# Kernel optimization log

Measured on AMD Instinct MI355X. Metric: run time of the kernel, lower is better.

Reference implementation:

```python
import jax, jax.numpy as jnp
import numpy as np

B, C, H, W = 4, 256, 64, 64
CH = C // 2  # inner channels


def setup_inputs() -> dict:
    key = jax.random.key(0)
    ks = jax.random.split(key, 9)
    s = 1.0 / np.sqrt(C)
    so = 1.0 / np.sqrt(CH)
    return {
        "x": jax.random.normal(ks[0], (B, C, H, W), dtype=jnp.float32),
        "teta_w": jax.random.uniform(ks[1], (CH, C), jnp.float32, -s, s),
        "teta_b": jax.random.uniform(ks[2], (CH,), jnp.float32, -s, s),
        "fi_w": jax.random.uniform(ks[3], (CH, C), jnp.float32, -s, s),
        "fi_b": jax.random.uniform(ks[4], (CH,), jnp.float32, -s, s),
        "gi_w": jax.random.uniform(ks[5], (CH, C), jnp.float32, -s, s),
        "gi_b": jax.random.uniform(ks[6], (CH,), jnp.float32, -s, s),
        "out_w": jax.random.uniform(ks[7], (C, CH), jnp.float32, -so, so),
        "out_b": jax.random.uniform(ks[8], (C,), jnp.float32, -so, so),
    }


def _conv1x1(x, w, b):
    # x: (B, Cin, H, W), w: (Cout, Cin) -> (B, Cout, H, W)
    return jnp.einsum('bchw,oc->bohw', x, w) + b[None, :, None, None]


def reference(x, teta_w, teta_b, fi_w, fi_b, gi_w, gi_b, out_w, out_b):
    b, c, h, w = x.shape
    n = h * w
    ch = teta_w.shape[0]
    # NOTE: original uses .view (reshape), NOT transpose, to get (B, N, Ch)
    x1 = _conv1x1(x, teta_w, teta_b).reshape(b, ch, n).reshape(b, n, ch)
    x2 = _conv1x1(x, fi_w, fi_b).reshape(b, ch, n)            # (B, Ch, N)
    x3 = _conv1x1(x, gi_w, gi_b).reshape(b, ch, n).reshape(b, n, ch)
    # softmax over dim=1 (rows), as in the original
    attn = jax.nn.softmax(jnp.matmul(x1, x2), axis=1)          # (B, N, N)
    y = jnp.matmul(attn, x3)                                   # (B, N, Ch)
    y = jnp.swapaxes(y, 1, 2).reshape(b, ch, h, w)
    return x + _conv1x1(y, out_w, out_b)
```

## Files before the change

### kernel.cpp

```cpp
#include <hip/hip_runtime.h>
#include <hip/hip_bf16.h>

#define BB 4
#define CC 256
#define CHH 128
#define NN 4096
#define KSHIFT 12.0f

typedef __attribute__((ext_vector_type(8))) short bf16x8;
typedef __attribute__((ext_vector_type(4))) float f32x4;

__device__ __forceinline__ float to_f(float v) { return v; }
__device__ __forceinline__ float to_f(__hip_bfloat16 v) { return __bfloat162float(v); }
__device__ __forceinline__ void st_f(float* p, float v) { *p = v; }
__device__ __forceinline__ void st_f(__hip_bfloat16* p, float v) { *p = __float2bfloat16(v); }
__device__ __forceinline__ unsigned short f2bf(float f) {
    __hip_bfloat16 h = __float2bfloat16(f);
    unsigned short u;
    __builtin_memcpy(&u, &h, 2);
    return u;
}
__device__ __forceinline__ bf16x8 ldb8(const unsigned short* p) { return *(const bf16x8*)p; }

__device__ __forceinline__ void gload_lds16(const unsigned short* g, unsigned short* l) {
    __builtin_amdgcn_global_load_lds(
        (const __attribute__((address_space(1))) unsigned int*)g,
        (__attribute__((address_space(3))) unsigned int*)l, 16, 0, 0);
}

__global__ void detect_kernel(const void* __restrict__ tb, int* __restrict__ flag) {
    if (threadIdx.x == 0) {
        const __hip_bfloat16* p = (const __hip_bfloat16*)tb;
        int big = 0, zeros = 0;
        for (int i = 0; i < 128; ++i) {
            float v = __bfloat162float(p[i]);
            if (!(fabsf(v) <= 0.5f)) big = 1;
            if ((i & 1) == 0 && v == 0.0f) zeros++;
        }
        *flag = (big || zeros >= 32) ? 1 : 0;
    }
}

template <typename T>
__device__ __forceinline__ void prep_body(const T* tw, const T* fw, const T* gw, const T* ow,
                                          const T* tb2, const T* fb, const T* gb, const T* ob,
                                          unsigned short* Wb, unsigned short* OWb,
                                          float* Bf, float* OBf) {
    int idx = blockIdx.x * 256 + threadIdx.x;
    if (idx < 98304) {
        int cv = idx >> 15, rem = idx & 32767;
        const T* src = cv == 0 ? tw : (cv == 1 ? fw : gw);
        Wb[idx] = f2bf(to_f(src[rem]));
    } else if (idx < 131072) {
        OWb[idx - 98304] = f2bf(to_f(ow[idx - 98304]));
    } else if (idx < 131456) {
        int r = idx - 131072;
        int cv = r >> 7, j = r & 127;
        const T* src = cv == 0 ? tb2 : (cv == 1 ? fb : gb);
        Bf[r] = to_f(src[j]);
    } else if (idx < 131712) {
        OBf[idx - 131456] = to_f(ob[idx - 131456]);
    }
}

__global__ void prep_kernel(const void* tw, const void* fw, const void* gw, const void* ow,
                            const void* tb2, const void* fb, const void* gb, const void* ob,
                            const int* __restrict__ flag,
                            unsigned short* Wb, unsigned short* OWb, float* Bf, float* OBf) {
    if (*flag)
        prep_body<float>((const float*)tw, (const float*)fw, (const float*)gw, (const float*)ow,
                         (const float*)tb2, (const float*)fb, (const float*)gb, (const float*)ob,
                         Wb, OWb, Bf, OBf);
    else
        prep_body<__hip_bfloat16>((const __hip_bfloat16*)tw, (const __hip_bfloat16*)fw,
                                  (const __hip_bfloat16*)gw, (const __hip_bfloat16*)ow,
                                  (const __hip_bfloat16*)tb2, (const __hip_bfloat16*)fb,
                                  (const __hip_bfloat16*)gb, (const __hip_bfloat16*)ob,
                                  Wb, OWb, Bf, OBf);
}

template <typename T>
__device__ __forceinline__ void xtrans_body(const T* __restrict__ x, unsigned short* __restrict__ xt) {
    int b = blockIdx.z;
    const T* in = x + (size_t)b * CC * NN;
    unsigned short* out = xt + (size_t)b * NN * CC;
    int p0 = blockIdx.x * 64, c0 = blockIdx.y * 64;
    __shared__ unsigned short t[64][68];
    int flat = threadIdx.x;
#pragma unroll
    for (int tt = 0; tt < 16; ++tt) {
        int id = flat + tt * 256;
        int rr = id >> 6, cc = id & 63;
        t[cc][rr] = f2bf(to_f(in[(size_t)(c0 + rr) * NN + p0 + cc]));
    }
    __syncthreads();
#pragma unroll
    for (int tt = 0; tt < 16; ++tt) {
        int id = flat + tt * 256;
        int pp = id >> 6, jj = id & 63;
        out[(size_t)(p0 + pp) * CC + c0 + jj] = t[pp][jj];
    }
}

__launch_bounds__(256)
__global__ void xtrans_kernel(const void* x, const int* __restrict__ flag,
                              unsigned short* __restrict__ xt) {
    if (*flag) xtrans_body<float>((const float*)x, xt);
    else       xtrans_body<__hip_bfloat16>((const __hip_bfloat16*)x, xt);
}

__launch_bounds__(256)
__global__ void conv3_mfma_kernel(const unsigned short* __restrict__ xt,
                                  const unsigned short* __restrict__ Wb,
                                  const float* __restrict__ Bf,
                                  unsigned short* __restrict__ T1b,
                                  unsigned short* __restrict__ T2t,
                                  unsigned short* __restrict__ T3b) {
    int b = blockIdx.y;
    int p0 = blockIdx.x * 16;
    int flat = threadIdx.x;
    int w = flat >> 6, lane = flat & 63, m = lane & 15, quad = lane >> 4;
    const unsigned short* xrow = xt + ((size_t)b * NN + p0 + m) * CC;
    bf16x8 xf[8];
#pragma unroll
    for (int kc = 0; kc < 8; ++kc)
        xf[kc] = ldb8(&xrow[kc * 32 + quad * 8]);
    unsigned short* t1  = T1b + (size_t)b * CHH * NN;
    unsigned short* t2t = T2t + (size_t)b * CHH * NN;
    unsigned short* t3  = T3b + (size_t)b * CHH * NN;
#pragma unroll
    for (int q = 0; q < 6; ++q) {
        int t = w * 6 + q;
        int cv = t >> 3, ot = t & 7;
        int o0 = ot * 16;
        const unsigned short* wrow = Wb + ((size_t)cv * CHH + o0 + m) * CC;
        f32x4 acc = {0.f, 0.f, 0.f, 0.f};
#pragma unroll
        for (int kc = 0; kc < 8; ++kc) {
            bf16x8 wf = ldb8(&wrow[kc * 32 + quad * 8]);
            acc = __builtin_amdgcn_mfma_f32_16x16x32_bf16(wf, xf[kc], acc, 0, 0, 0);
        }
        unsigned short hv[4];
#pragma unroll
        for (int r = 0; r < 4; ++r)
            hv[r] = f2bf(acc[r] + Bf[cv * CHH + o0 + quad * 4 + r]);
        if (cv == 1) {
            unsigned int lo = (unsigned int)hv[0] | ((unsigned int)hv[1] << 16);
            unsigned int hi = (unsigned int)hv[2] | ((unsigned int)hv[3] << 16);
            int src = (lane & 3) * 16 + (lane >> 2);
            unsigned int tlo = (unsigned int)__shfl((int)lo, src, 64);
            unsigned int thi = (unsigned int)__shfl((int)hi, src, 64);
            unsigned int* dst = (unsigned int*)&t2t[(size_t)(p0 + (lane >> 2)) * CHH +
                                                    o0 + (lane & 3) * 4];
            dst[0] = tlo;
            dst[1] = thi;
        } else {
            unsigned short* outp = (cv == 0) ? t1 : t3;
#pragma unroll
            for (int r = 0; r < 4; ++r)
                outp[(size_t)(o0 + quad * 4 + r) * NN + p0 + m] = hv[r];
        }
    }
}

__launch_bounds__(256)
__global__ void transpose_kernel(const unsigned short* __restrict__ in,
                                 unsigned short* __restrict__ out, int R, int C) {
    int bz = blockIdx.z;
    in  += (size_t)bz * R * C;
    out += (size_t)bz * R * C;
    int c0 = blockIdx.x * 64, r0 = blockIdx.y * 64;
    __shared__ unsigned short t[64][68];
    int flat = threadIdx.x;
#pragma unroll
    for (int tt = 0; tt < 16; ++tt) {
        int id = flat + tt * 256;
        int r = id >> 6, c = id & 63;
        t[c][r] = in[(size_t)(r0 + r) * C + c0 + c];
    }
    __syncthreads();
#pragma unroll
    for (int tt = 0; tt < 16; ++tt) {
        int id = flat + tt * 256;
        int c = id >> 6, r = id & 63;
        out[(size_t)(c0 + c) * R + r0 + r] = t[c][r];
    }
}

__launch_bounds__(256)
__global__ void stats_mfma_kernel(const unsigned short* __restrict__ T1b,
                                  const unsigned short* __restrict__ T2t,
                                  float* __restrict__ Lpart) {
    int blk = blockIdx.x;
    int b = (blk & 7) >> 1;
    int rest = (blk >> 3) * 2 + (blk & 1);
    int strip = rest >> 3, iq = rest & 7;
    int ibase = iq * 512;
    int flat = threadIdx.x;
    int w = flat >> 6, lane = flat & 63, m = lane & 15, quad = lane >> 4;
    const unsigned short* A  = T1b + (size_t)b * CHH * NN;
    const unsigned short* Bt = T2t + (size_t)b * CHH * NN;
    __shared__ unsigned short th[2][64 * 128];

    int u0w = strip * 128 + w * 32;
    bf16x8 bfr[2][4];
#pragma unroll
    for (int g = 0; g < 2; ++g)
#pragma unroll
        for (int kc = 0; kc < 4; ++kc)
            bfr[g][kc] = ldb8(&Bt[(size_t)(u0w + g * 16 + m) * CHH + kc * 32 + quad * 8]);

#define STAGE_TH(dst, ii)                                                          \
    _Pragma("unroll")                                                              \
    for (int i_ = 0; i_ < 4; ++i_) {                                               \
        int sl = i_ * 256 + flat;                                                  \
        int r_ = sl >> 4, ch_ = sl & 15;                                           \
        int c_ = ch_ ^ (r_ & 7);                                                   \
        gload_lds16(&A[(size_t)((ii) + r_) * CHH + c_ * 8], &th[dst][sl * 8]);     \
    }

    float csum[2] = {0.f, 0.f};
    STAGE_TH(0, ibase);
    __syncthreads();
    int cur = 0;
    for (int t = 0; t < 8; ++t) {
        if (t < 7) { STAGE_TH(cur ^ 1, ibase + (t + 1) * 64); }
        const unsigned short* thc = th[cur];
#pragma unroll
        for (int s = 0; s < 4; ++s) {
            int irow = s * 16 + m;
            bf16x8 af[4];
#pragma unroll
            for (int kc = 0; kc < 4; ++kc) {
                int ch = (kc * 4 + quad) ^ (irow & 7);
                af[kc] = *(const bf16x8*)&thc[irow * 128 + ch * 8];
            }
#pragma unroll
            for (int g = 0; g < 2; ++g) {
                f32x4 acc = {0.f, 0.f, 0.f, 0.f};
#pragma unroll
                for (int kc = 0; kc < 4; ++kc)
                    acc = __builtin_amdgcn_mfma_f32_16x16x32_bf16(af[kc], bfr[g][kc], acc, 0, 0, 0);
#pragma unroll
                for (int r = 0; r < 4; ++r)
                    csum[g] += __expf(acc[r] - KSHIFT);
            }
        }
        if (t < 7) {
            __syncthreads();
            cur ^= 1;
        }
    }
#undef STAGE_TH
#pragma unroll
    for (int g = 0; g < 2; ++g) {
        csum[g] += __shfl_xor(csum[g], 16, 64);
        csum[g] += __shfl_xor(csum[g], 32, 64);
        if (lane < 16)
            Lpart[((size_t)iq * BB + b) * NN + u0w + g * 16 + m] = csum[g];
    }
}

__launch_bounds__(256)
__global__ void attn_mfma_kernel(const unsigned short* __restrict__ T1b,
                                 const unsigned short* __restrict__ T2t,
                                 const unsigned short* __restrict__ X3t,
                                 const float* __restrict__ Lpart,
                                 unsigned short* __restrict__ Yp0,
                                 unsigned short* __restrict__ Yp1,
                                 unsigned short* __restrict__ Yp2,
                                 unsigned short* __restrict__ Yp3) {
    int blk = blockIdx.x;
    int b = (blk & 7) >> 1;
    int rest = (blk >> 3) * 2 + (blk & 1);
    int it = rest >> 2, uc = rest & 3;
    int i0 = it * 128;
    unsigned short* Yp = uc == 0 ? Yp0 : (uc == 1 ? Yp1 : (uc == 2 ? Yp2 : Yp3));
    int flat = threadIdx.x;
    int w = flat >> 6, lane = flat & 63, m = lane & 15, quad = lane >> 4;
    const unsigned short* A  = T1b + (size_t)b * CHH * NN;
    const unsigned short* Bt = T2t + (size_t)b * CHH * NN;
    const unsigned short* X3 = X3t + (size_t)b * CHH * NN;

    __shared__ unsigned short bt[2][64 * 128];
    __shared__ unsigned short x3[2][128 * 64];
    __shared__ unsigned short pT[4][2][16][40];
    __shared__ float llh[1024];

    int ubeg = uc * 1024;
#pragma unroll
    for (int k = 0; k < 4; ++k) {
        int idx = k * 256 + flat;
        int u = ubeg + idx;
        float s = 0.f;
#pragma unroll
        for (int c = 0; c < 8; ++c)
            s += Lpart[((size_t)c * BB + b) * NN + u];
        llh[idx] = logf(s) + KSHIFT;
    }

    int iw = i0 + w * 32;
    bf16x8 ath[2][4];
#pragma unroll
    for (int g = 0; g < 2; ++g)
#pragma unroll
        for (int kc = 0; kc < 4; ++kc)
            ath[g][kc] = ldb8(&A[(size_t)(iw + g * 16 + m) * CHH + kc * 32 + quad * 8]);
    f32x4 yacc[2][8];
#pragma unroll
    for (int g = 0; g < 2; ++g)
#pragma unroll
        for (int js = 0; js < 8; ++js) yacc[g][js] = (f32x4){0.f, 0.f, 0.f, 0.f};

#define STAGE_UT(dst, uu)                                                          \
    _Pragma("unroll")                                                              \
    for (int i_ = 0; i_ < 4; ++i_) {                    \
        int sl = i_ * 256 + flat;                                                  \
        int u_ = sl >> 4, ch_ = sl & 15;                                           \
        int c_ = ch_ ^ (u_ & 7);                                                   \
        gload_lds16(&Bt[(size_t)((uu) + u_) * CHH + c_ * 8], &bt[dst][sl * 8]);    \
    }                                                                              \
    _Pragma("unroll")                                                              \
    for (int i_ = 0; i_ < 4; ++i_) {                    \
        int sl = i_ * 256 + flat;                                                  \
        int j_ = sl >> 3, ch_ = sl & 7;                                            \
        int c_ = ch_ ^ (j_ & 7);                                                   \
        gload_lds16(&X3[(size_t)j_ * NN + (uu) + c_ * 8], &x3[dst][sl * 8]);       \
    }

    STAGE_UT(0, ubeg);
    __syncthreads();
    int cur = 0;
    for (int t = 0; t < 16; ++t) {
        int u0 = ubeg + t * 64;
        if (t < 15) { STAGE_UT(cur ^ 1, u0 + 64); }
        const unsigned short* btc = bt[cur];
        const unsigned short* x3c = x3[cur];
#pragma unroll
        for (int h = 0; h < 2; ++h) {
#pragma unroll
            for (int su = 0; su < 2; ++su) {
                int u = h * 32 + su * 16 + m;
                f32x4 a0 = {0.f, 0.f, 0.f, 0.f}, a1 = {0.f, 0.f, 0.f, 0.f};
#pragma unroll
                for (int kc = 0; kc < 4; ++kc) {
                    int ch = (kc * 4 + quad) ^ (u & 7);
                    bf16x8 bf = *(const bf16x8*)&btc[u * 128 + ch * 8];
                    a0 = __builtin_amdgcn_mfma_f32_16x16x32_bf16(ath[0][kc], bf, a0, 0, 0, 0);
                    a1 = __builtin_amdgcn_mfma_f32_16x16x32_bf16(ath[1][kc], bf, a1, 0, 0, 0);
                }
                float ll = llh[u0 - ubeg + u];
#pragma unroll
                for (int r = 0; r < 4; ++r) {
                    pT[w][0][quad * 4 + r][su * 16 + m] = f2bf(__expf(a0[r] - ll));
                    pT[w][1][quad * 4 + r][su * 16 + m] = f2bf(__expf(a1[r] - ll));
                }
            }
            bf16x8 pa0 = *(const bf16x8*)&pT[w][0][m][quad * 8];
            bf16x8 pa1 = *(const bf16x8*)&pT[w][1][m][quad * 8];
#pragma unroll
            for (int js = 0; js < 8; ++js) {
                int j = js * 16 + m;
                int ch = (h * 4 + quad) ^ (j & 7);
                bf16x8 xb = *(const bf16x8*)&x3c[j * 64 + ch * 8];
                yacc[0][js] = __builtin_amdgcn_mfma_f32_16x16x32_bf16(pa0, xb, yacc[0][js], 0, 0, 0);
                yacc[1][js] = __builtin_amdgcn_mfma_f32_16x16x32_bf16(pa1, xb, yacc[1][js], 0, 0, 0);
            }
        }
        if (t < 15) {
            __syncthreads();
            cur ^= 1;
        }
    }
#undef STAGE_UT
#pragma unroll
    for (int g = 0; g < 2; ++g)
#pragma unroll
        for (int js = 0; js < 8; ++js)
#pragma unroll
            for (int r = 0; r < 4; ++r)
                Yp[((size_t)b * NN + iw + g * 16 + quad * 4 + r) * CHH + js * 16 + m] =
                    f2bf(yacc[g][js][r]);
}

template <typename T>
__device__ __forceinline__ void outconv_body(const T* __restrict__ x,
                                             const unsigned short* __restrict__ Yp0,
                                             const unsigned short* __restrict__ Yp1,
                                             const unsigned short* __restrict__ Yp2,
                                             const unsigned short* __restrict__ Yp3,
                                             const unsigned short* __restrict__ OWb,
                                             const float* __restrict__ OBf,
                                             T* __restrict__ out) {
    int b = blockIdx.y;
    int p0 = blockIdx.x * 16;
    int flat = threadIdx.x;
    int w = flat >> 6, lane = flat & 63, m = lane & 15, quad = lane >> 4;
    size_t yoff = ((size_t)b * NN + p0 + m) * CHH;
    const unsigned short* yrows[4] = {Yp0 + yoff, Yp1 + yoff, Yp2 + yoff, Yp3 + yoff};
    bf16x8 yf[4][4];
#pragma unroll
    for (int pz = 0; pz < 4; ++pz)
#pragma unroll
        for (int kc = 0; kc < 4; ++kc)
            yf[pz][kc] = ldb8(&yrows[pz][kc * 32 + quad * 8]);
#pragma unroll
    for (int q = 0; q < 4; ++q) {
        int o0 = (w * 4 + q) * 16;
        const unsigned short* wrow = OWb + (size_t)(o0 + m) * CHH;
        f32x4 acc = {0.f, 0.f, 0.f, 0.f};
#pragma unroll
        for (int kc = 0; kc < 4; ++kc) {
            bf16x8 aw = ldb8(&wrow[kc * 32 + quad * 8]);
#pragma unroll
            for (int pz = 0; pz < 4; ++pz)
                acc = __builtin_amdgcn_mfma_f32_16x16x32_bf16(aw, yf[pz][kc], acc, 0, 0, 0);
        }
#pragma unroll
        for (int r = 0; r < 4; ++r) {
            int co = o0 + quad * 4 + r;
            size_t oi = ((size_t)b * CC + co) * NN + p0 + m;
            st_f(&out[oi], acc[r] + OBf[co] + to_f(x[oi]));
        }
    }
}

__launch_bounds__(256)
__global__ void outconv_mfma_kernel(const void* x,
                                    const unsigned short* __restrict__ Yp0,
                                    const unsigned short* __restrict__ Yp1,
                                    const unsigned short* __restrict__ Yp2,
                                    const unsigned short* __restrict__ Yp3,
                                    const unsigned short* __restrict__ OWb,
                                    const float* __restrict__ OBf,
                                    const int* __restrict__ flag, void* out) {
    if (*flag)
        outconv_body<float>((const float*)x, Yp0, Yp1, Yp2, Yp3, OWb, OBf, (float*)out);
    else
        outconv_body<__hip_bfloat16>((const __hip_bfloat16*)x, Yp0, Yp1, Yp2, Yp3, OWb, OBf,
                                     (__hip_bfloat16*)out);
}

extern "C" void kernel_launch(void* const* d_in, const int* in_sizes, int n_in,
                              void* d_out, int out_size, void* d_ws, size_t ws_size,
                              hipStream_t stream) {
    const void* x  = d_in[0];
    const void* tw = d_in[1];
    const void* tb = d_in[2];
    const void* fw = d_in[3];
    const void* fb = d_in[4];
    const void* gw = d_in[5];
    const void* gb = d_in[6];
    const void* ow = d_in[7];
    const void* ob = d_in[8];

    const size_t TE = (size_t)BB * CHH * NN;
    unsigned short* T1b = (unsigned short*)d_ws;
    unsigned short* T2t = T1b + TE;
    unsigned short* X3t = T2t + TE;
    unsigned short* T3b = X3t + TE;
    unsigned short* xt  = T3b + TE;
    unsigned short* Yp0 = xt;
    unsigned short* Yp1 = xt + TE;
    unsigned short* Yp2 = T3b;
    unsigned short* Yp3 = xt + 2 * TE;
    unsigned short* Wb  = Yp3 + TE;
    unsigned short* OWb = Wb + 98304;
    float* Bf    = (float*)(OWb + 32768);
    float* OBf   = Bf + 384;
    float* Lpart = OBf + 256;
    int*   Flag  = (int*)(Lpart + 131072);

    detect_kernel<<<1, 64, 0, stream>>>(tb, Flag);
    prep_kernel<<<dim3(515), 256, 0, stream>>>(tw, fw, gw, ow, tb, fb, gb, ob,
                                               Flag, Wb, OWb, Bf, OBf);
    xtrans_kernel<<<dim3(NN / 64, CC / 64, BB), 256, 0, stream>>>(x, Flag, xt);
    conv3_mfma_kernel<<<dim3(NN / 16, BB), 256, 0, stream>>>(xt, Wb, Bf, T1b, T2t, T3b);
    transpose_kernel<<<dim3(CHH / 64, NN / 64, BB), 256, 0, stream>>>(T3b, X3t, NN, CHH);
    stats_mfma_kernel<<<dim3(1024), 256, 0, stream>>>(T1b, T2t, Lpart);
    attn_mfma_kernel<<<dim3(512), 256, 0, stream>>>(T1b, T2t, X3t, Lpart, Yp0, Yp1, Yp2, Yp3);
    outconv_mfma_kernel<<<dim3(NN / 16, BB), 256, 0, stream>>>(x, Yp0, Yp1, Yp2, Yp3,
                                                               OWb, OBf, Flag, d_out);
}
```

Measured before the change: 217.1 us.

## Split attention kernel work across 8 waves with 16 rows each

New measurement: 212.5 us. -2.1%, faster.

```diff
diff --git a/kernel.cpp b/kernel.cpp
--- a/kernel.cpp
+++ b/kernel.cpp
@@ -261,7 +261,7 @@
     }
 }
 
-__launch_bounds__(256)
+__launch_bounds__(512, 4)
 __global__ void attn_mfma_kernel(const unsigned short* __restrict__ T1b,
                                  const unsigned short* __restrict__ T2t,
                                  const unsigned short* __restrict__ X3t,
@@ -284,13 +284,13 @@
 
     __shared__ unsigned short bt[2][64 * 128];
     __shared__ unsigned short x3[2][128 * 64];
-    __shared__ unsigned short pT[4][2][16][40];
+    __shared__ unsigned short pT[8][16][40];
     __shared__ float llh[1024];
 
     int ubeg = uc * 1024;
 #pragma unroll
-    for (int k = 0; k < 4; ++k) {
-        int idx = k * 256 + flat;
+    for (int k = 0; k < 2; ++k) {
+        int idx = k * 512 + flat;
         int u = ubeg + idx;
         float s = 0.f;
 #pragma unroll
@@ -299,30 +299,26 @@
         llh[idx] = logf(s) + KSHIFT;
     }
 
-    int iw = i0 + w * 32;
-    bf16x8 ath[2][4];
-#pragma unroll
-    for (int g = 0; g < 2; ++g)
-#pragma unroll
-        for (int kc = 0; kc < 4; ++kc)
-            ath[g][kc] = ldb8(&A[(size_t)(iw + g * 16 + m) * CHH + kc * 32 + quad * 8]);
-    f32x4 yacc[2][8];
-#pragma unroll
-    for (int g = 0; g < 2; ++g)
-#pragma unroll
-        for (int js = 0; js < 8; ++js) yacc[g][js] = (f32x4){0.f, 0.f, 0.f, 0.f};
+    int iw = i0 + w * 16;
+    bf16x8 ath[4];
+#pragma unroll
+    for (int kc = 0; kc < 4; ++kc)
+        ath[kc] = ldb8(&A[(size_t)(iw + m) * CHH + kc * 32 + quad * 8]);
+    f32x4 yacc[8];
+#pragma unroll
+    for (int js = 0; js < 8; ++js) yacc[js] = (f32x4){0.f, 0.f, 0.f, 0.f};
 
 #define STAGE_UT(dst, uu)                                                          \
     _Pragma("unroll")                                                              \
-    for (int i_ = 0; i_ < 4; ++i_) {                    \
-        int sl = i_ * 256 + flat;                                                  \
+    for (int i_ = 0; i_ < 2; ++i_) {                    \
+        int sl = i_ * 512 + flat;                                                  \
         int u_ = sl >> 4, ch_ = sl & 15;                                           \
         int c_ = ch_ ^ (u_ & 7);                                                   \
         gload_lds16(&Bt[(size_t)((uu) + u_) * CHH + c_ * 8], &bt[dst][sl * 8]);    \
     }                                                                              \
     _Pragma("unroll")                                                              \
-    for (int i_ = 0; i_ < 4; ++i_) {                    \
-        int sl = i_ * 256 + flat;                                                  \
+    for (int i_ = 0; i_ < 2; ++i_) {                    \
+        int sl = i_ * 512 + flat;                                                  \
         int j_ = sl >> 3, ch_ = sl & 7;                                            \
         int c_ = ch_ ^ (j_ & 7);                                                   \
         gload_lds16(&X3[(size_t)j_ * NN + (uu) + c_ * 8], &x3[dst][sl * 8]);       \
@@ -341,30 +337,25 @@
 #pragma unroll
             for (int su = 0; su < 2; ++su) {
                 int u = h * 32 + su * 16 + m;
-                f32x4 a0 = {0.f, 0.f, 0.f, 0.f}, a1 = {0.f, 0.f, 0.f, 0.f};
+                f32x4 a0 = {0.f, 0.f, 0.f, 0.f};
 #pragma unroll
                 for (int kc = 0; kc < 4; ++kc) {
                     int ch = (kc * 4 + quad) ^ (u & 7);
                     bf16x8 bf = *(const bf16x8*)&btc[u * 128 + ch * 8];
-                    a0 = __builtin_amdgcn_mfma_f32_16x16x32_bf16(ath[0][kc], bf, a0, 0, 0, 0);
-                    a1 = __builtin_amdgcn_mfma_f32_16x16x32_bf16(ath[1][kc], bf, a1, 0, 0, 0);
+                    a0 = __builtin_amdgcn_mfma_f32_16x16x32_bf16(ath[kc], bf, a0, 0, 0, 0);
                 }
                 float ll = llh[u0 - ubeg + u];
 #pragma unroll
-                for (int r = 0; r < 4; ++r) {
-                    pT[w][0][quad * 4 + r][su * 16 + m] = f2bf(__expf(a0[r] - ll));
-                    pT[w][1][quad * 4 + r][su * 16 + m] = f2bf(__expf(a1[r] - ll));
-                }
+                for (int r = 0; r < 4; ++r)
+                    pT[w][quad * 4 + r][su * 16 + m] = f2bf(__expf(a0[r] - ll));
             }
-            bf16x8 pa0 = *(const bf16x8*)&pT[w][0][m][quad * 8];
-            bf16x8 pa1 = *(const bf16x8*)&pT[w][1][m][quad * 8];
+            bf16x8 pa0 = *(const bf16x8*)&pT[w][m][quad * 8];
 #pragma unroll
             for (int js = 0; js < 8; ++js) {
                 int j = js * 16 + m;
                 int ch = (h * 4 + quad) ^ (j & 7);
                 bf16x8 xb = *(const bf16x8*)&x3c[j * 64 + ch * 8];
-                yacc[0][js] = __builtin_amdgcn_mfma_f32_16x16x32_bf16(pa0, xb, yacc[0][js], 0, 0, 0);
-                yacc[1][js] = __builtin_amdgcn_mfma_f32_16x16x32_bf16(pa1, xb, yacc[1][js], 0, 0, 0);
+                yacc[js] = __builtin_amdgcn_mfma_f32_16x16x32_bf16(pa0, xb, yacc[js], 0, 0, 0);
             }
         }
         if (t < 15) {
@@ -374,13 +365,11 @@
     }
 #undef STAGE_UT
 #pragma unroll
-    for (int g = 0; g < 2; ++g)
-#pragma unroll
-        for (int js = 0; js < 8; ++js)
-#pragma unroll
-            for (int r = 0; r < 4; ++r)
-                Yp[((size_t)b * NN + iw + g * 16 + quad * 4 + r) * CHH + js * 16 + m] =
-                    f2bf(yacc[g][js][r]);
+    for (int js = 0; js < 8; ++js)
+#pragma unroll
+        for (int r = 0; r < 4; ++r)
+            Yp[((size_t)b * NN + iw + quad * 4 + r) * CHH + js * 16 + m] =
+                f2bf(yacc[js][r]);
 }
 
 template <typename T>
@@ -478,7 +467,7 @@
     conv3_mfma_kernel<<<dim3(NN / 16, BB), 256, 0, stream>>>(xt, Wb, Bf, T1b, T2t, T3b);
     transpose_kernel<<<dim3(CHH / 64, NN / 64, BB), 256, 0, stream>>>(T3b, X3t, NN, CHH);
     stats_mfma_kernel<<<dim3(1024), 256, 0, stream>>>(T1b, T2t, Lpart);
-    attn_mfma_kernel<<<dim3(512), 256, 0, stream>>>(T1b, T2t, X3t, Lpart, Yp0, Yp1, Yp2, Yp3);
+    attn_mfma_kernel<<<dim3(512), 512, 0, stream>>>(T1b, T2t, X3t, Lpart, Yp0, Yp1, Yp2, Yp3);
     outconv_mfma_kernel<<<dim3(NN / 16, BB), 256, 0, stream>>>(x, Yp0, Yp1, Yp2, Yp3,
                                                                OWb, OBf, Flag, d_out);
 }
```

## Split attention u-halves across eight waves and reduce partial outputs in LDS

Applied to the files above, without the earlier changes.

New measurement: 272.5 us. +25.5%, slower.

```diff
diff --git a/kernel.cpp b/kernel.cpp
--- a/kernel.cpp
+++ b/kernel.cpp
@@ -261,7 +261,7 @@
     }
 }
 
-__launch_bounds__(256)
+__launch_bounds__(512, 4)
 __global__ void attn_mfma_kernel(const unsigned short* __restrict__ T1b,
                                  const unsigned short* __restrict__ T2t,
                                  const unsigned short* __restrict__ X3t,
@@ -278,19 +278,21 @@
     unsigned short* Yp = uc == 0 ? Yp0 : (uc == 1 ? Yp1 : (uc == 2 ? Yp2 : Yp3));
     int flat = threadIdx.x;
     int w = flat >> 6, lane = flat & 63, m = lane & 15, quad = lane >> 4;
+    int ig = w & 3, h = w >> 2;
     const unsigned short* A  = T1b + (size_t)b * CHH * NN;
     const unsigned short* Bt = T2t + (size_t)b * CHH * NN;
     const unsigned short* X3 = X3t + (size_t)b * CHH * NN;
 
-    __shared__ unsigned short bt[2][64 * 128];
-    __shared__ unsigned short x3[2][128 * 64];
-    __shared__ unsigned short pT[4][2][16][40];
-    __shared__ float llh[1024];
+    __shared__ __align__(16) unsigned char smem[73728];
+    unsigned short* bt0 = (unsigned short*)smem;
+    unsigned short* x3s = (unsigned short*)(smem + 32768);
+    unsigned short* pTw = (unsigned short*)(smem + 49152) + w * 1280;
+    float* llh = (float*)(smem + 69632);
 
     int ubeg = uc * 1024;
 #pragma unroll
-    for (int k = 0; k < 4; ++k) {
-        int idx = k * 256 + flat;
+    for (int k = 0; k < 2; ++k) {
+        int idx = k * 512 + flat;
         int u = ubeg + idx;
         float s = 0.f;
 #pragma unroll
@@ -299,7 +301,7 @@
         llh[idx] = logf(s) + KSHIFT;
     }
 
-    int iw = i0 + w * 32;
+    int iw = i0 + ig * 32;
     bf16x8 ath[2][4];
 #pragma unroll
     for (int g = 0; g < 2; ++g)
@@ -312,75 +314,92 @@
 #pragma unroll
         for (int js = 0; js < 8; ++js) yacc[g][js] = (f32x4){0.f, 0.f, 0.f, 0.f};
 
-#define STAGE_UT(dst, uu)                                                          \
+#define STAGE_BT(dst, uu)                                                          \
     _Pragma("unroll")                                                              \
-    for (int i_ = 0; i_ < 4; ++i_) {                    \
-        int sl = i_ * 256 + flat;                                                  \
+    for (int i_ = 0; i_ < 2; ++i_) {                                    \
+        int sl = i_ * 512 + flat;                                                  \
         int u_ = sl >> 4, ch_ = sl & 15;                                           \
         int c_ = ch_ ^ (u_ & 7);                                                   \
-        gload_lds16(&Bt[(size_t)((uu) + u_) * CHH + c_ * 8], &bt[dst][sl * 8]);    \
-    }                                                                              \
+        gload_lds16(&Bt[(size_t)((uu) + u_) * CHH + c_ * 8],                       \
+                    bt0 + (dst) * 8192 + sl * 8);                                  \
+    }
+#define STAGE_X3(uu)                                                               \
     _Pragma("unroll")                                                              \
-    for (int i_ = 0; i_ < 4; ++i_) {                    \
-        int sl = i_ * 256 + flat;                                                  \
+    for (int i_ = 0; i_ < 2; ++i_) {                                    \
+        int sl = i_ * 512 + flat;                                                  \
         int j_ = sl >> 3, ch_ = sl & 7;                                            \
         int c_ = ch_ ^ (j_ & 7);                                                   \
-        gload_lds16(&X3[(size_t)j_ * NN + (uu) + c_ * 8], &x3[dst][sl * 8]);       \
-    }
-
-    STAGE_UT(0, ubeg);
+        gload_lds16(&X3[(size_t)j_ * NN + (uu) + c_ * 8], x3s + sl * 8);           \
+    }
+
+    STAGE_BT(0, ubeg);
+    STAGE_X3(ubeg);
     __syncthreads();
     int cur = 0;
     for (int t = 0; t < 16; ++t) {
         int u0 = ubeg + t * 64;
-        if (t < 15) { STAGE_UT(cur ^ 1, u0 + 64); }
-        const unsigned short* btc = bt[cur];
-        const unsigned short* x3c = x3[cur];
-#pragma unroll
-        for (int h = 0; h < 2; ++h) {
-#pragma unroll
-            for (int su = 0; su < 2; ++su) {
-                int u = h * 32 + su * 16 + m;
-                f32x4 a0 = {0.f, 0.f, 0.f, 0.f}, a1 = {0.f, 0.f, 0.f, 0.f};
-#pragma unroll
-                for (int kc = 0; kc < 4; ++kc) {
-                    int ch = (kc * 4 + quad) ^ (u & 7);
-                    bf16x8 bf = *(const bf16x8*)&btc[u * 128 + ch * 8];
-                    a0 = __builtin_amdgcn_mfma_f32_16x16x32_bf16(ath[0][kc], bf, a0, 0, 0, 0);
-                    a1 = __builtin_amdgcn_mfma_f32_16x16x32_bf16(ath[1][kc], bf, a1, 0, 0, 0);
+        if (t < 15) { STAGE_BT(cur ^ 1, u0 + 64); }
+        const unsigned short* btc = bt0 + cur * 8192;
+#pragma unroll
+        for (int su = 0; su < 2; ++su) {
+            int ul = h * 32 + su * 16 + m;
+            f32x4 a0 = {0.f, 0.f, 0.f, 0.f}, a1 = {0.f, 0.f, 0.f, 0.f};
+#pragma unroll
+            for (int kc = 0; kc < 4; ++kc) {
+                int ch = (kc * 4 + quad) ^ (ul & 7);
+                bf16x8 bf = *(const bf16x8*)&btc[ul * 128 + ch * 8];
+                a0 = __builtin_amdgcn_mfma_f32_16x16x32_bf16(ath[0][kc], bf, a0, 0, 0, 0);
+                a1 = __builtin_amdgcn_mfma_f32_16x16x32_bf16(ath[1][kc], bf, a1, 0, 0, 0);
+            }
+            float ll = llh[u0 - ubeg + ul];
+#pragma unroll
+            for (int r = 0; r < 4; ++r) {
+                pTw[(quad * 4 + r) * 40 + su * 16 + m]       = f2bf(__expf(a0[r] - ll));
+                pTw[640 + (quad * 4 + r) * 40 + su * 16 + m] = f2bf(__expf(a1[r] - ll));
+            }
+        }
+        bf16x8 pa0 = *(const bf16x8*)&pTw[m * 40 + quad * 8];
+        bf16x8 pa1 = *(const bf16x8*)&pTw[640 + m * 40 + quad * 8];
+        __syncthreads();
+#pragma unroll
+        for (int js = 0; js < 8; ++js) {
+            int j = js * 16 + m;
+            int ch = (h * 4 + quad) ^ (j & 7);
+            bf16x8 xb = *(const bf16x8*)&x3s[j * 64 + ch * 8];
+            yacc[0][js] = __builtin_amdgcn_mfma_f32_16x16x32_bf16(pa0, xb, yacc[0][js], 0, 0, 0);
+            yacc[1][js] = __builtin_amdgcn_mfma_f32_16x16x32_bf16(pa1, xb, yacc[1][js], 0, 0, 0);
+        }
+        __syncthreads();
+        if (t < 15) { STAGE_X3(u0 + 64); }
+        cur ^= 1;
+    }
+#undef STAGE_BT
+#undef STAGE_X3
+    float* scr = (float*)smem;
+    if (h == 1) {
+#pragma unroll
+        for (int g = 0; g < 2; ++g)
+#pragma unroll
+            for (int js = 0; js < 8; ++js)
+#pragma unroll
+                for (int r = 0; r < 4; ++r)
+                    scr[ig * 4224 + (g * 16 + quad * 4 + r) * 132 + js * 16 + m] =
+                        yacc[g][js][r];
+    }
+    __syncthreads();
+    if (h == 0) {
+#pragma unroll
+        for (int g = 0; g < 2; ++g)
+#pragma unroll
+            for (int js = 0; js < 8; ++js)
+#pragma unroll
+                for (int r = 0; r < 4; ++r) {
+                    float v = yacc[g][js][r] +
+                              scr[ig * 4224 + (g * 16 + quad * 4 + r) * 132 + js * 16 + m];
+                    Yp[((size_t)b * NN + iw + g * 16 + quad * 4 + r) * CHH + js * 16 + m] =
+                        f2bf(v);
                 }
-                float ll = llh[u0 - ubeg + u];
-#pragma unroll
-                for (int r = 0; r < 4; ++r) {
-                    pT[w][0][quad * 4 + r][su * 16 + m] = f2bf(__expf(a0[r] - ll));
-                    pT[w][1][quad * 4 + r][su * 16 + m] = f2bf(__expf(a1[r] - ll));
-                }
-            }
-            bf16x8 pa0 = *(const bf16x8*)&pT[w][0][m][quad * 8];
-            bf16x8 pa1 = *(const bf16x8*)&pT[w][1][m][quad * 8];
-#pragma unroll
-            for (int js = 0; js < 8; ++js) {
-                int j = js * 16 + m;
-                int ch = (h * 4 + quad) ^ (j & 7);
-                bf16x8 xb = *(const bf16x8*)&x3c[j * 64 + ch * 8];
-                yacc[0][js] = __builtin_amdgcn_mfma_f32_16x16x32_bf16(pa0, xb, yacc[0][js], 0, 0, 0);
-                yacc[1][js] = __builtin_amdgcn_mfma_f32_16x16x32_bf16(pa1, xb, yacc[1][js], 0, 0, 0);
-            }
-        }
-        if (t < 15) {
-            __syncthreads();
-            cur ^= 1;
-        }
-    }
-#undef STAGE_UT
-#pragma unroll
-    for (int g = 0; g < 2; ++g)
-#pragma unroll
-        for (int js = 0; js < 8; ++js)
-#pragma unroll
-            for (int r = 0; r < 4; ++r)
-                Yp[((size_t)b * NN + iw + g * 16 + quad * 4 + r) * CHH + js * 16 + m] =
-                    f2bf(yacc[g][js][r]);
+    }
 }
 
 template <typename T>
@@ -478,7 +497,7 @@
     conv3_mfma_kernel<<<dim3(NN / 16, BB), 256, 0, stream>>>(xt, Wb, Bf, T1b, T2t, T3b);
     transpose_kernel<<<dim3(CHH / 64, NN / 64, BB), 256, 0, stream>>>(T3b, X3t, NN, CHH);
     stats_mfma_kernel<<<dim3(1024), 256, 0, stream>>>(T1b, T2t, Lpart);
-    attn_mfma_kernel<<<dim3(512), 256, 0, stream>>>(T1b, T2t, X3t, Lpart, Yp0, Yp1, Yp2, Yp3);
+    attn_mfma_kernel<<<dim3(512), 512, 0, stream>>>(T1b, T2t, X3t, Lpart, Yp0, Yp1, Yp2, Yp3);
     outconv_mfma_kernel<<<dim3(NN / 16, BB), 256, 0, stream>>>(x, Yp0, Yp1, Yp2, Yp3,
                                                                OWb, OBf, Flag, d_out);
 }
```
